# Optimization experiments

Measured on AMD Instinct MI355X. Metric: run time of the kernel, lower is better.

The kernel has to match this reference:

```python
import jax, jax.numpy as jnp
import numpy as np

H = 768      # hidden_size
NH = 12      # num_heads
HD = H // NH # head_dim = 64


def setup_inputs() -> dict:
    key = jax.random.key(0)
    k1, k2, k3 = jax.random.split(key, 3)
    x = jax.random.normal(k1, (4, 2048, H), dtype=jnp.float32)
    # nn.Linear weights are [out, in]; we store transposed [in, out] for x @ W
    w_qkv = jax.random.normal(k2, (H, 3 * H), dtype=jnp.float32) * (1.0 / np.sqrt(H))
    w_out = jax.random.normal(k3, (H, H), dtype=jnp.float32) * (1.0 / np.sqrt(H))
    return {"x": x, "w_qkv": w_qkv, "w_out": w_out}


def reference(x, w_qkv, w_out):
    B, S, _ = x.shape
    qkv = (x @ w_qkv).reshape(B, S, 3, NH, HD)
    qkv = jnp.transpose(qkv, (2, 0, 3, 1, 4))  # [3, B, NH, S, HD]
    q, k, v = qkv[0], qkv[1], qkv[2]
    scale = 1.0 / np.sqrt(HD)
    scores = jnp.einsum('bhqd,bhkd->bhqk', q, k) * scale  # [B,NH,S,S]
    causal = jnp.tril(jnp.ones((S, S), dtype=bool))
    scores = jnp.where(causal, scores, jnp.finfo(scores.dtype).min)
    attn = jax.nn.softmax(scores, axis=-1)
    out = jnp.einsum('bhqk,bhkd->bhqd', attn, v)          # [B,NH,S,HD]
    out = jnp.transpose(out, (0, 2, 1, 3)).reshape(B, S, H)
    return out @ w_out
```

## Files before the change

kernel.cpp:

```cpp
#include <hip/hip_runtime.h>
#include <type_traits>

#define S_LEN 2048
#define HID   768
#define NHEAD 12
#define HDIM  64
#define BATCH 4

typedef __attribute__((ext_vector_type(4))) float float4v;
typedef __attribute__((ext_vector_type(8))) short short8;
typedef __attribute__((ext_vector_type(4))) short short4v;
typedef __attribute__((ext_vector_type(2))) int int2v;

__device__ __forceinline__ short f2b(float f) {
  unsigned u = __float_as_uint(f);
  u += 0x7fff + ((u >> 16) & 1);
  return (short)(u >> 16);
}

__device__ __forceinline__ unsigned pkbf(float a, float b) {
#if __has_builtin(__builtin_amdgcn_cvt_pk_bf16_f32)
  typedef __attribute__((ext_vector_type(2))) __bf16 bf2;
  bf2 r = __builtin_amdgcn_cvt_pk_bf16_f32(a, b);
  return *(unsigned*)&r;
#else
  return ((unsigned)(unsigned short)f2b(a)) |
         (((unsigned)(unsigned short)f2b(b)) << 16);
#endif
}

__device__ __forceinline__ float fexp2(float x) {
#if __has_builtin(__builtin_amdgcn_exp2f)
  return __builtin_amdgcn_exp2f(x);
#else
  return __expf(x * 0.69314718056f);
#endif
}

__device__ __forceinline__ void g2l16(const short* g, short* l) {
  __builtin_amdgcn_global_load_lds(
      (const __attribute__((address_space(1))) void*)g,
      (__attribute__((address_space(3))) void*)l, 16, 0, 0);
}

__global__ __launch_bounds__(256) void prepass(const float* __restrict__ x,
                                               const float* __restrict__ w_qkv,
                                               const float* __restrict__ w_out,
                                               short* __restrict__ xb,
                                               short* __restrict__ wqkvT,
                                               short* __restrict__ woutT) {
  __shared__ float tile[64][65];
  const int blk = blockIdx.x;
  if (blk < 3072) {
    int i = blk * 2048 + threadIdx.x * 8;
    float4v a = *(const float4v*)&x[i];
    float4v b = *(const float4v*)&x[i + 4];
    short8 o;
#pragma unroll
    for (int j = 0; j < 4; j++) { o[j] = f2b(a[j]); o[j + 4] = f2b(b[j]); }
    *(short8*)&xb[i] = o;
    return;
  }
  const float* W; short* WT; int N_, scaleN, idx;
  if (blk < 3504) { idx = blk - 3072; W = w_qkv; WT = wqkvT; N_ = 3 * HID; scaleN = HID; }
  else            { idx = blk - 3504; W = w_out; WT = woutT; N_ = HID;     scaleN = 0;  }
  const int nblk = N_ / 64;
  const int n0 = (idx % nblk) * 64, k0 = (idx / nblk) * 64;
  const int tx = threadIdx.x & 63, ty = threadIdx.x >> 6;
#pragma unroll
  for (int r = 0; r < 16; r++) {
    int row = r * 4 + ty;
    tile[row][tx] = W[(size_t)(k0 + row) * N_ + n0 + tx];
  }
  __syncthreads();
#pragma unroll
  for (int r = 0; r < 16; r++) {
    int row = r * 4 + ty;
    float sc = (n0 + row < scaleN) ? 0.18033688011f : 1.0f;
    WT[(size_t)(n0 + row) * HID + k0 + tx] = f2b(tile[tx][row] * sc);
  }
}

template <int OUT>
__global__ __launch_bounds__(256) void gemm_bt(const short* __restrict__ A,
                                               const short* __restrict__ Bt,
                                               float* __restrict__ Cf,
                                               short* __restrict__ Cq,
                                               short* __restrict__ vT,
                                               int M, int N, int K) {
  __shared__ __align__(16) short As[2][128 * 32];
  __shared__ __align__(16) short Bs[2][128 * 32];
  const int tid = threadIdx.x;
  const int w = tid >> 6, lane = tid & 63;
  const int quad = lane >> 4, lm = lane & 15;

  const int gx = gridDim.x;
  const int nwg = gx * gridDim.y;
  int flat = blockIdx.y * gx + blockIdx.x;
  if ((nwg & 7) == 0) flat = (flat & 7) * (nwg >> 3) + (flat >> 3);
  const int m0 = (flat / gx) * 128, n0 = (flat % gx) * 128;
  const int mo = (w & 1) * 64, no = (w >> 1) * 64;

  float4v acc[4][4];
#pragma unroll
  for (int i = 0; i < 4; i++)
#pragma unroll
    for (int j = 0; j < 4; j++) acc[i][j] = (float4v)0.0f;

  const int srow = w * 32 + (lane >> 2);
  const int scol = (lane & 3) * 8;
  const short* Ag = A + (size_t)(m0 + srow) * K + scol;
  const short* Bg = Bt + (size_t)(n0 + srow) * K + scol;

  for (int kb = 0; kb < K; kb += 64) {
#pragma unroll
    for (int s = 0; s < 2; s++) {
      short* Al = &As[s][(w * 32) * 32];
      short* Bl = &Bs[s][(w * 32) * 32];
      g2l16(Ag + kb + s * 32, Al);
      g2l16(Ag + kb + s * 32 + (size_t)16 * K, Al + 16 * 32);
      g2l16(Bg + kb + s * 32, Bl);
      g2l16(Bg + kb + s * 32 + (size_t)16 * K, Bl + 16 * 32);
    }
    __syncthreads();

#pragma unroll
    for (int s = 0; s < 2; s++) {
      short8 af[4], bf[4];
#pragma unroll
      for (int i = 0; i < 4; i++)
        af[i] = *(const short8*)&As[s][(mo + i * 16 + lm) * 32 + quad * 8];
#pragma unroll
      for (int j = 0; j < 4; j++)
        bf[j] = *(const short8*)&Bs[s][(no + j * 16 + lm) * 32 + quad * 8];
#pragma unroll
      for (int i = 0; i < 4; i++)
#pragma unroll
        for (int j = 0; j < 4; j++)
          acc[i][j] = __builtin_amdgcn_mfma_f32_16x16x32_bf16(af[i], bf[j], acc[i][j], 0, 0, 0);
    }
    __syncthreads();
  }

  if constexpr (OUT == 0) {
#pragma unroll
    for (int i = 0; i < 4; i++)
#pragma unroll
      for (int j = 0; j < 4; j++)
#pragma unroll
        for (int r = 0; r < 4; r++)
          Cf[(size_t)(m0 + mo + i * 16 + quad * 4 + r) * N + n0 + no + j * 16 + lm] =
              acc[i][j][r];
  } else {
    if (n0 >= 2 * HID) {
      const int b = m0 >> 11;
      const int s0 = (m0 & 2047) + mo + quad * 4;
#pragma unroll
      for (int i = 0; i < 4; i++)
#pragma unroll
        for (int j = 0; j < 4; j++) {
          int col = n0 + no + j * 16 + lm - 2 * HID;
          int h = col >> 6, d = col & 63;
          short4v pv;
#pragma unroll
          for (int r = 0; r < 4; r++) pv[r] = f2b(acc[i][j][r]);
          *(short4v*)&vT[((size_t)(b * NHEAD + h) * HDIM + d) * S_LEN + s0 + i * 16] = pv;
        }
    } else {
#pragma unroll
      for (int i = 0; i < 4; i++)
#pragma unroll
        for (int j = 0; j < 4; j++)
#pragma unroll
          for (int r = 0; r < 4; r++)
            Cq[(size_t)(m0 + mo + i * 16 + quad * 4 + r) * (2 * HID) + n0 + no + j * 16 + lm] =
                f2b(acc[i][j][r]);
    }
  }
}

__global__ __launch_bounds__(256) void attn_mfma(const short* __restrict__ qk,
                                                 const short* __restrict__ vT,
                                                 short* __restrict__ attnout) {
  __shared__ __align__(16) short Ks[2][64 * 64];
  __shared__ __align__(16) short Vt[2][64 * 64];
  __shared__ __align__(16) short Ps[4][16 * 64];

  const int tid = threadIdx.x;
  const int w = tid >> 6, lane = tid & 63;
  const int quad = lane >> 4, lm = lane & 15;
  const int bh = blockIdx.x, a = blockIdx.y;
  const int b = bh / NHEAD, h = bh % NHEAD;
  const int qtile[2] = {a, 31 - a};

  short8 aq[2][2];
#pragma unroll
  for (int t = 0; t < 2; t++)
#pragma unroll
    for (int kb = 0; kb < 2; kb++)
      aq[t][kb] = *(const short8*)&qk[(size_t)(b * S_LEN + qtile[t] * 64 + w * 16 + lm) * (2 * HID) +
                                      h * HDIM + kb * 32 + quad * 8];

  const float4v z4 = (float4v)0.0f;
  short8 one8;
#pragma unroll
  for (int j = 0; j < 8; j++) one8[j] = (short)0x3F80;

  const size_t kbase = (size_t)(b * S_LEN) * (2 * HID) + HID + h * HDIM;
  const size_t vbase = (size_t)(b * NHEAD + h) * HDIM * S_LEN;
  const short* kptr[2];
  const short* vptr[2];
#pragma unroll
  for (int i = 0; i < 2; i++) {
    int c = (w * 2 + i) * 64 + lane;
    int row = c >> 3, slot = c & 7;
    int q8 = slot ^ (row & 7);
    int key = 4 * (row & 15) + (row >> 4);
    kptr[i] = qk + kbase + (size_t)key * (2 * HID) + q8 * 8;
    vptr[i] = vT + vbase + (size_t)row * S_LEN + q8 * 8;
  }

#define ISSUE(BUF)                                                    \
  {                                                                   \
    _Pragma("unroll") for (int i = 0; i < 2; i++) {                   \
      g2l16(kptr[i], &Ks[BUF][(w * 2 + i) * 512]);                    \
      g2l16(vptr[i], &Vt[BUF][(w * 2 + i) * 512]);                    \
      kptr[i] += 64 * 2 * HID;                                        \
      vptr[i] += 64;                                                  \
    }                                                                 \
  }

  const int swx = (lm & 7) << 4;
  const int loff0 = (quad * 16) ^ swx;
  const int loff1 = (64 + quad * 16) ^ swx;
  const int rowK = lm << 7;
  const char* KsB = (const char*)&Ks[0][0];
  const char* VtB = (const char*)&Vt[0][0];
  const char* PsW = (const char*)&Ps[w][0];
  const char* pread0 = PsW + rowK + loff0;
  const char* pread1 = PsW + rowK + loff1;
  char* pswa[4];
#pragma unroll
  for (int r = 0; r < 4; r++) {
    int rowp = quad * 4 + r;
    pswa[r] = (char*)PsW + (rowp << 7) + ((lm * 8) ^ ((rowp & 7) << 4));
  }

  float4v o_acc[2][4];
#pragma unroll
  for (int t = 0; t < 2; t++)
#pragma unroll
    for (int nt = 0; nt < 4; nt++) o_acc[t][nt] = (float4v)0.0f;
  float4v o1[2];
  o1[0] = (float4v)0.0f;
  o1[1] = (float4v)0.0f;

  const int ktmax = 32 - a;
  int cur = 0;

  ISSUE(0);

  for (int kt = 0; kt < ktmax; kt++) {
    asm volatile("s_waitcnt vmcnt(0)" ::: "memory");
    __syncthreads();
    if (kt + 1 < ktmax) ISSUE(cur ^ 1);

    const int coff = cur << 13;
    const char* kB0 = KsB + coff + rowK + loff0;
    const char* kB1 = KsB + coff + rowK + loff1;
    const char* vB0 = VtB + coff + rowK + loff0;
    const char* vB1 = VtB + coff + rowK + loff1;

#pragma unroll
    for (int t = 0; t < 2; t++) {
      if (t == 0 && kt > a) continue;
      float4v s_acc[4];
      __builtin_amdgcn_s_setprio(1);
#pragma unroll
      for (int nt = 0; nt < 4; nt++) {
        short8 bk = *(const short8*)(kB0 + nt * 2048);
        s_acc[nt] = __builtin_amdgcn_mfma_f32_16x16x32_bf16(aq[t][0], bk, z4, 0, 0, 0);
      }
#pragma unroll
      for (int nt = 0; nt < 4; nt++) {
        short8 bk = *(const short8*)(kB1 + nt * 2048);
        s_acc[nt] = __builtin_amdgcn_mfma_f32_16x16x32_bf16(aq[t][1], bk, s_acc[nt], 0, 0, 0);
      }
      __builtin_amdgcn_s_setprio(0);

      const bool diag = (kt == qtile[t]);
#pragma unroll
      for (int r = 0; r < 4; r++) {
        float e[4];
#pragma unroll
        for (int nt = 0; nt < 4; nt++) {
          float v = fexp2(s_acc[nt][r]);
          if (diag && (4 * lm + nt > w * 16 + quad * 4 + r)) v = 0.0f;
          e[nt] = v;
        }
        int2v p2 = {(int)pkbf(e[0], e[1]), (int)pkbf(e[2], e[3])};
        *(int2v*)pswa[r] = p2;
      }

      __builtin_amdgcn_s_setprio(1);
#pragma unroll
      for (int kb = 0; kb < 2; kb++) {
        short8 ap = *(const short8*)(kb ? pread1 : pread0);
        const char* vB = kb ? vB1 : vB0;
        o1[t] = __builtin_amdgcn_mfma_f32_16x16x32_bf16(ap, one8, o1[t], 0, 0, 0);
#pragma unroll
        for (int nt = 0; nt < 4; nt++) {
          short8 bv = *(const short8*)(vB + nt * 2048);
          o_acc[t][nt] = __builtin_amdgcn_mfma_f32_16x16x32_bf16(ap, bv, o_acc[t][nt], 0, 0, 0);
        }
      }
      __builtin_amdgcn_s_setprio(0);
    }
    cur ^= 1;
  }

#pragma unroll
  for (int t = 0; t < 2; t++)
#pragma unroll
    for (int r = 0; r < 4; r++) {
      float inv = 1.0f / o1[t][r];
      int rowg = b * S_LEN + qtile[t] * 64 + w * 16 + quad * 4 + r;
#pragma unroll
      for (int nt = 0; nt < 4; nt++)
        attnout[(size_t)rowg * HID + h * HDIM + nt * 16 + lm] =
            f2b(o_acc[t][nt][r] * inv);
    }
#undef ISSUE
}

extern "C" void kernel_launch(void* const* d_in, const int* in_sizes, int n_in,
                              void* d_out, int out_size, void* d_ws, size_t ws_size,
                              hipStream_t stream) {
  const float* x     = (const float*)d_in[0];
  const float* w_qkv = (const float*)d_in[1];
  const float* w_out = (const float*)d_in[2];
  float* out = (float*)d_out;

  const int M = BATCH * S_LEN;
  short* qk     = (short*)d_ws;
  short* attn   = qk + (size_t)M * 2 * HID;
  short* vT     = attn + (size_t)M * HID;
  short* xb     = vT + (size_t)M * HID;
  short* wqkvT  = xb + (size_t)M * HID;
  short* woutT  = wqkvT + (size_t)(3 * HID) * HID;

  prepass<<<3648, 256, 0, stream>>>(x, w_qkv, w_out, xb, wqkvT, woutT);

  gemm_bt<1><<<dim3(3 * HID / 128, M / 128), 256, 0, stream>>>(
      xb, wqkvT, nullptr, qk, vT, M, 3 * HID, HID);
  attn_mfma<<<dim3(BATCH * NHEAD, S_LEN / 128), 256, 0, stream>>>(qk, vT, attn);
  gemm_bt<0><<<dim3(HID / 128, M / 128), 256, 0, stream>>>(
      attn, woutT, out, nullptr, nullptr, M, HID, HID);
}
```

Baseline: 193.6 us.

## Double-buffer GEMM K-loop with prefetch and swap MFMA operands for V-transpose store

Restructures the GEMM main loop from load-then-compute over two 32-wide halves into a double-buffered pipeline. The next 32-wide K tile is prefetched into the alternate LDS buffer while the current one feeds the MFMAs, and MFMA issue priority is raised with s_setprio. For V-tiles the MFMA operands are swapped so each accumulator holds the transposed result, and the vT store becomes scalar per-element writes with lanes spanning the sequence dimension for coalescing. This aims to overlap global-to-LDS loads with compute and to improve the transposed store pattern, at the cost of a barrier per 32-wide step and a templated dual loop.

```diff
diff --git a/kernel.cpp b/kernel.cpp
--- a/kernel.cpp
+++ b/kernel.cpp
@@ -112,35 +112,53 @@
   const short* Ag = A + (size_t)(m0 + srow) * K + scol;
   const short* Bg = Bt + (size_t)(n0 + srow) * K + scol;
 
-  for (int kb = 0; kb < K; kb += 64) {
-#pragma unroll
-    for (int s = 0; s < 2; s++) {
-      short* Al = &As[s][(w * 32) * 32];
-      short* Bl = &Bs[s][(w * 32) * 32];
-      g2l16(Ag + kb + s * 32, Al);
-      g2l16(Ag + kb + s * 32 + (size_t)16 * K, Al + 16 * 32);
-      g2l16(Bg + kb + s * 32, Bl);
-      g2l16(Bg + kb + s * 32 + (size_t)16 * K, Bl + 16 * 32);
+#define STAGE(KT, BUF)                                           \
+  {                                                              \
+    short* Al = &As[BUF][(w * 32) * 32];                         \
+    short* Bl = &Bs[BUF][(w * 32) * 32];                         \
+    const short* ag = Ag + (KT) * 32;                            \
+    const short* bg = Bg + (KT) * 32;                            \
+    g2l16(ag, Al);                                               \
+    g2l16(ag + (size_t)16 * K, Al + 16 * 32);                    \
+    g2l16(bg, Bl);                                               \
+    g2l16(bg + (size_t)16 * K, Bl + 16 * 32);                    \
+  }
+
+  const bool vsw = (OUT == 1) && (n0 >= 2 * HID);
+  const int nkt = K / 32;
+
+  auto kloop = [&](auto vswc) {
+    constexpr bool VSW = decltype(vswc)::value;
+    int cur = 0;
+    STAGE(0, 0);
+    for (int kt = 0; kt < nkt; ++kt) {
+      asm volatile("s_waitcnt vmcnt(0)" ::: "memory");
+      __syncthreads();
+      if (kt + 1 < nkt) STAGE(kt + 1, cur ^ 1);
+      short8 af[4], bf[4];
+#pragma unroll
+      for (int i = 0; i < 4; i++)
+        af[i] = *(const short8*)&As[cur][(mo + i * 16 + lm) * 32 + quad * 8];
+#pragma unroll
+      for (int j = 0; j < 4; j++)
+        bf[j] = *(const short8*)&Bs[cur][(no + j * 16 + lm) * 32 + quad * 8];
+      __builtin_amdgcn_s_setprio(1);
+#pragma unroll
+      for (int i = 0; i < 4; i++)
+#pragma unroll
+        for (int j = 0; j < 4; j++) {
+          if constexpr (VSW)
+            acc[i][j] = __builtin_amdgcn_mfma_f32_16x16x32_bf16(bf[j], af[i], acc[i][j], 0, 0, 0);
+          else
+            acc[i][j] = __builtin_amdgcn_mfma_f32_16x16x32_bf16(af[i], bf[j], acc[i][j], 0, 0, 0);
+        }
+      __builtin_amdgcn_s_setprio(0);
+      cur ^= 1;
     }
-    __syncthreads();
-
-#pragma unroll
-    for (int s = 0; s < 2; s++) {
-      short8 af[4], bf[4];
-#pragma unroll
-      for (int i = 0; i < 4; i++)
-        af[i] = *(const short8*)&As[s][(mo + i * 16 + lm) * 32 + quad * 8];
-#pragma unroll
-      for (int j = 0; j < 4; j++)
-        bf[j] = *(const short8*)&Bs[s][(no + j * 16 + lm) * 32 + quad * 8];
-#pragma unroll
-      for (int i = 0; i < 4; i++)
-#pragma unroll
-        for (int j = 0; j < 4; j++)
-          acc[i][j] = __builtin_amdgcn_mfma_f32_16x16x32_bf16(af[i], bf[j], acc[i][j], 0, 0, 0);
-    }
-    __syncthreads();
-  }
+  };
+  if (vsw) kloop(std::true_type{});
+  else     kloop(std::false_type{});
+#undef STAGE
 
   if constexpr (OUT == 0) {
 #pragma unroll
@@ -154,18 +172,19 @@
   } else {
     if (n0 >= 2 * HID) {
       const int b = m0 >> 11;
-      const int s0 = (m0 & 2047) + mo + quad * 4;
-#pragma unroll
-      for (int i = 0; i < 4; i++)
+#pragma unroll
+      for (int i = 0; i < 4; i++) {
+        const int sG = (m0 & 2047) + mo + i * 16 + lm;
 #pragma unroll
         for (int j = 0; j < 4; j++) {
-          int col = n0 + no + j * 16 + lm - 2 * HID;
-          int h = col >> 6, d = col & 63;
-          short4v pv;
-#pragma unroll
-          for (int r = 0; r < 4; r++) pv[r] = f2b(acc[i][j][r]);
-          *(short4v*)&vT[((size_t)(b * NHEAD + h) * HDIM + d) * S_LEN + s0 + i * 16] = pv;
+#pragma unroll
+          for (int r = 0; r < 4; r++) {
+            int nG = n0 + no + j * 16 + quad * 4 + r - 2 * HID;
+            int h = nG >> 6, d = nG & 63;
+            vT[((size_t)(b * NHEAD + h) * HDIM + d) * S_LEN + sG] = f2b(acc[i][j][r]);
+          }
         }
+      }
     } else {
 #pragma unroll
       for (int i = 0; i < 4; i++)
```

Result: slower. 205.3 us (+6.0%).

## Swizzle GEMM LDS layout and split V projection into transposed-output GEMM

Applied to the files above, without the earlier changes.

XOR-swizzles the LDS column placement for both A and B tiles in the GEMM, on the write and read sides, to reduce bank conflicts on the fragment reads. The QKV projection is split into two launches: a Q/K GEMM writing row-major bf16, and a separate V GEMM (OUT==2) that swaps the MFMA operands so the accumulator comes out transposed. Each lane then holds consecutive sequence positions for writing vT. This removes the runtime branch inside the kernel but adds a kernel launch, and the new vT store writes scalar shorts instead of 4-wide vectors.

```diff
diff --git a/kernel.cpp b/kernel.cpp
--- a/kernel.cpp
+++ b/kernel.cpp
@@ -108,9 +108,11 @@
     for (int j = 0; j < 4; j++) acc[i][j] = (float4v)0.0f;
 
   const int srow = w * 32 + (lane >> 2);
-  const int scol = (lane & 3) * 8;
+  const int scol = ((lane & 3) ^ ((lane >> 3) & 3)) * 8;
   const short* Ag = A + (size_t)(m0 + srow) * K + scol;
   const short* Bg = Bt + (size_t)(n0 + srow) * K + scol;
+
+  const int qsw8 = (quad ^ ((lm >> 1) & 3)) * 8;
 
   for (int kb = 0; kb < K; kb += 64) {
 #pragma unroll
@@ -129,15 +131,19 @@
       short8 af[4], bf[4];
 #pragma unroll
       for (int i = 0; i < 4; i++)
-        af[i] = *(const short8*)&As[s][(mo + i * 16 + lm) * 32 + quad * 8];
+        af[i] = *(const short8*)&As[s][(mo + i * 16 + lm) * 32 + qsw8];
 #pragma unroll
       for (int j = 0; j < 4; j++)
-        bf[j] = *(const short8*)&Bs[s][(no + j * 16 + lm) * 32 + quad * 8];
+        bf[j] = *(const short8*)&Bs[s][(no + j * 16 + lm) * 32 + qsw8];
 #pragma unroll
       for (int i = 0; i < 4; i++)
 #pragma unroll
-        for (int j = 0; j < 4; j++)
-          acc[i][j] = __builtin_amdgcn_mfma_f32_16x16x32_bf16(af[i], bf[j], acc[i][j], 0, 0, 0);
+        for (int j = 0; j < 4; j++) {
+          if constexpr (OUT == 2)
+            acc[i][j] = __builtin_amdgcn_mfma_f32_16x16x32_bf16(bf[j], af[i], acc[i][j], 0, 0, 0);
+          else
+            acc[i][j] = __builtin_amdgcn_mfma_f32_16x16x32_bf16(af[i], bf[j], acc[i][j], 0, 0, 0);
+        }
     }
     __syncthreads();
   }
@@ -151,30 +157,29 @@
         for (int r = 0; r < 4; r++)
           Cf[(size_t)(m0 + mo + i * 16 + quad * 4 + r) * N + n0 + no + j * 16 + lm] =
               acc[i][j][r];
+  } else if constexpr (OUT == 1) {
+#pragma unroll
+    for (int i = 0; i < 4; i++)
+#pragma unroll
+      for (int j = 0; j < 4; j++)
+#pragma unroll
+        for (int r = 0; r < 4; r++)
+          Cq[(size_t)(m0 + mo + i * 16 + quad * 4 + r) * (2 * HID) + n0 + no + j * 16 + lm] =
+              f2b(acc[i][j][r]);
   } else {
-    if (n0 >= 2 * HID) {
-      const int b = m0 >> 11;
-      const int s0 = (m0 & 2047) + mo + quad * 4;
-#pragma unroll
-      for (int i = 0; i < 4; i++)
-#pragma unroll
-        for (int j = 0; j < 4; j++) {
-          int col = n0 + no + j * 16 + lm - 2 * HID;
+    const int b = m0 >> 11;
+#pragma unroll
+    for (int i = 0; i < 4; i++) {
+      const int sG = (m0 & 2047) + mo + i * 16 + lm;
+#pragma unroll
+      for (int j = 0; j < 4; j++) {
+#pragma unroll
+        for (int r = 0; r < 4; r++) {
+          int col = n0 + no + j * 16 + quad * 4 + r;
           int h = col >> 6, d = col & 63;
-          short4v pv;
-#pragma unroll
-          for (int r = 0; r < 4; r++) pv[r] = f2b(acc[i][j][r]);
-          *(short4v*)&vT[((size_t)(b * NHEAD + h) * HDIM + d) * S_LEN + s0 + i * 16] = pv;
+          vT[((size_t)(b * NHEAD + h) * HDIM + d) * S_LEN + sG] = f2b(acc[i][j][r]);
         }
-    } else {
-#pragma unroll
-      for (int i = 0; i < 4; i++)
-#pragma unroll
-        for (int j = 0; j < 4; j++)
-#pragma unroll
-          for (int r = 0; r < 4; r++)
-            Cq[(size_t)(m0 + mo + i * 16 + quad * 4 + r) * (2 * HID) + n0 + no + j * 16 + lm] =
-                f2b(acc[i][j][r]);
+      }
     }
   }
 }
@@ -351,8 +356,10 @@
 
   prepass<<<3648, 256, 0, stream>>>(x, w_qkv, w_out, xb, wqkvT, woutT);
 
-  gemm_bt<1><<<dim3(3 * HID / 128, M / 128), 256, 0, stream>>>(
-      xb, wqkvT, nullptr, qk, vT, M, 3 * HID, HID);
+  gemm_bt<1><<<dim3(2 * HID / 128, M / 128), 256, 0, stream>>>(
+      xb, wqkvT, nullptr, qk, nullptr, M, 2 * HID, HID);
+  gemm_bt<2><<<dim3(HID / 128, M / 128), 256, 0, stream>>>(
+      xb, wqkvT + (size_t)(2 * HID) * HID, nullptr, nullptr, vT, M, HID, HID);
   attn_mfma<<<dim3(BATCH * NHEAD, S_LEN / 128), 256, 0, stream>>>(qk, vT, attn);
   gemm_bt<0><<<dim3(HID / 128, M / 128), 256, 0, stream>>>(
       attn, woutT, out, nullptr, nullptr, M, HID, HID);
```

Result: no change. 194.4 us (+0.4%).
